# Performance work log

Measured on AMD Instinct MI355X. Metric: run time of the kernel, lower is better.

Reference implementation:

```python
import jax, jax.numpy as jnp
import numpy as np

# config constants
H = 1024          # hidden_size
I = 512           # moe_intermediate_size
IS = 1024         # moe_shared_expert_intermediate_size
E = 16            # n_routed_experts
G = 4             # n_group
TOPK_G = 2        # topk_group
TOPK = 4          # num_experts_per_tok
SCALE = 2.5       # routed_scaling_factor
B, S = 2, 1024


def _relu2(x):
    r = jax.nn.relu(x)
    return r * r


def setup_inputs() -> dict:
    key = jax.random.key(0)
    ks = jax.random.split(key, 8)
    sd = 0.02
    return {
        "hidden_states": jax.random.normal(ks[0], (B, S, H), jnp.float32),
        "Wg": jax.random.normal(ks[1], (E, H), jnp.float32) * sd,          # router gate weight
        "bias_corr": jax.random.normal(ks[2], (E,), jnp.float32) * 0.01,    # e_score_correction_bias
        "W1": jax.random.normal(ks[3], (E, I, H), jnp.float32) * sd,        # experts up_proj
        "W2": jax.random.normal(ks[4], (E, H, I), jnp.float32) * sd,        # experts down_proj
        "Ws1": jax.random.normal(ks[5], (IS, H), jnp.float32) * sd,         # shared up_proj
        "Ws2": jax.random.normal(ks[6], (H, IS), jnp.float32) * sd,         # shared down_proj
    }


def _route(scores, bias_corr):
    # scores: (T,E) = sigmoid(router logits)
    T = scores.shape[0]
    s_choice = scores + bias_corr                                           # (T,E)
    gs = s_choice.reshape(T, G, E // G)
    group_scores = jnp.sum(jax.lax.top_k(gs, 2)[0], axis=-1)                # (T,G) sum of top-2 per group
    gidx = jax.lax.top_k(group_scores, TOPK_G)[1]                           # (T,topk_group)
    gmask = jnp.sum(jax.nn.one_hot(gidx, G, dtype=scores.dtype), axis=1)    # (T,G)
    smask = jnp.repeat(gmask, E // G, axis=1)                               # (T,E)
    masked = jnp.where(smask > 0, s_choice, 0.0)
    topk_idx = jax.lax.top_k(masked, TOPK)[1]                               # (T,top_k)
    topk_w = jnp.take_along_axis(scores, topk_idx, axis=1)                  # weights from raw sigmoid scores
    topk_w = topk_w / (jnp.sum(topk_w, axis=-1, keepdims=True) + 1e-20)     # norm_topk_prob
    topk_w = topk_w * SCALE
    return topk_idx, topk_w


def reference(hidden_states, Wg, bias_corr, W1, W2, Ws1, Ws2):
    b, s, h = hidden_states.shape
    flat = hidden_states.reshape(-1, h)                                     # (T,H)
    T = flat.shape[0]
    logits = flat.astype(jnp.float32) @ Wg.T                                # (T,E)
    scores = jax.nn.sigmoid(logits)
    topk_idx, topk_w = _route(scores, bias_corr)
    topk_w = topk_w.astype(hidden_states.dtype)
    # combined per-(token, expert) weight; zero where not routed (equivalent
    # to the per-expert gather/MLP/weighted index_add in the original)
    cw = jnp.zeros((T, E), flat.dtype)
    cw = cw.at[jnp.arange(T)[:, None], topk_idx].add(topk_w)                # (T,E)
    # fc1_latent_proj / fc2_latent_proj are Identity (moe_latent_size=None)
    hid = _relu2(jnp.einsum('th,eih->eti', flat, W1))                       # (E,T,I)
    y = jnp.einsum('eti,ehi->eth', hid, W2)                                 # (E,T,H)
    out = jnp.einsum('eth,te->th', y, cw)                                   # (T,H)
    shared = _relu2(flat @ Ws1.T) @ Ws2.T                                   # shared expert on residuals
    return (out + shared).reshape(b, s, h)
```

## Files before the change

kernel.cpp:

```cpp
#include <hip/hip_runtime.h>
#include <hip/hip_bf16.h>

#define T_TOK 2048
#define HDIM 1024
#define IDIM 512
#define ISDIM 1024
#define NEXP 16
#define TOPK 4
#define NSLOT (T_TOK*TOPK)
#define SCALE_F 2.5f

typedef unsigned short u16;
typedef float f32x4 __attribute__((ext_vector_type(4)));
typedef __bf16 bf16x8 __attribute__((ext_vector_type(8)));
typedef u16 u16x8 __attribute__((ext_vector_type(8)));

__device__ __forceinline__ u16 f2bf(float f) {
  unsigned u = __builtin_bit_cast(unsigned, f);
  u += 0x7fffu + ((u >> 16) & 1u);
  return (u16)(u >> 16);
}

__device__ __forceinline__ float bf2f(u16 h) {
  unsigned u = ((unsigned)h) << 16;
  return __builtin_bit_cast(float, u);
}

__device__ __forceinline__ void gload_lds16(const u16* g, u16* l) {
  __builtin_amdgcn_global_load_lds(
      (const __attribute__((address_space(1))) void*)g,
      (__attribute__((address_space(3))) void*)l, 16, 0, 0);
}

__device__ __forceinline__ f32x4 mfma16(u16x8 a, u16x8 b, f32x4 c) {
  return __builtin_amdgcn_mfma_f32_16x16x32_bf16(
      __builtin_bit_cast(bf16x8, a), __builtin_bit_cast(bf16x8, b), c, 0, 0, 0);
}

__device__ __forceinline__ void wait_vm6()   { asm volatile("s_waitcnt vmcnt(6)" ::: "memory"); }
__device__ __forceinline__ void wait_vm0()   { asm volatile("s_waitcnt vmcnt(0)" ::: "memory"); }
__device__ __forceinline__ void wait_lgkm0() { asm volatile("s_waitcnt lgkmcnt(0)" ::: "memory"); }

__global__ void __launch_bounds__(256) router_kernel(
    const float* __restrict__ x, const float* __restrict__ Wg,
    const float* __restrict__ bias,
    int* __restrict__ topk_idx, float* __restrict__ topk_w,
    u16* __restrict__ Xbf) {
  int t = blockIdx.x;
  int tid = threadIdx.x;
  int lane = tid & 63;
  int wave = tid >> 6;

  __shared__ __align__(16) float sx[HDIM];
  __shared__ float ssc[NEXP];

  float4 xv = reinterpret_cast<const float4*>(x + (size_t)t * HDIM)[tid];
  reinterpret_cast<float4*>(sx)[tid] = xv;
  ushort4 o;
  o.x = f2bf(xv.x); o.y = f2bf(xv.y); o.z = f2bf(xv.z); o.w = f2bf(xv.w);
  reinterpret_cast<ushort4*>(Xbf + (size_t)t * HDIM)[tid] = o;
  __syncthreads();

  float acc[4] = {0.f, 0.f, 0.f, 0.f};
  const float4* sx4 = reinterpret_cast<const float4*>(sx);
#pragma unroll
  for (int c = 0; c < 4; c++) {
    float4 xq = sx4[lane + 64 * c];
#pragma unroll
    for (int e = 0; e < 4; e++) {
      float4 wq = reinterpret_cast<const float4*>(
          Wg + (size_t)(wave * 4 + e) * HDIM)[lane + 64 * c];
      acc[e] += xq.x * wq.x + xq.y * wq.y + xq.z * wq.z + xq.w * wq.w;
    }
  }
#pragma unroll
  for (int e = 0; e < 4; e++) {
    float v = acc[e];
#pragma unroll
    for (int off = 32; off > 0; off >>= 1) v += __shfl_xor(v, off);
    if (lane == 0) ssc[wave * 4 + e] = v;
  }
  __syncthreads();

  if (tid == 0) {
    float scores[NEXP], sc[NEXP];
#pragma unroll
    for (int e = 0; e < NEXP; e++) {
      float s = 1.f / (1.f + expf(-ssc[e]));
      scores[e] = s;
      sc[e] = s + bias[e];
    }
    float gsum[4];
#pragma unroll
    for (int g = 0; g < 4; g++) {
      float a = sc[4*g], b = sc[4*g+1], c = sc[4*g+2], d = sc[4*g+3];
      float hi1 = fmaxf(a, b), lo1 = fminf(a, b);
      float hi2 = fmaxf(c, d), lo2 = fminf(c, d);
      gsum[g] = fmaxf(hi1, hi2) + fmaxf(fminf(hi1, hi2), fmaxf(lo1, lo2));
    }
    int g0 = 0; float bv = gsum[0];
#pragma unroll
    for (int g = 1; g < 4; g++) if (gsum[g] > bv) { bv = gsum[g]; g0 = g; }
    int g1 = -1; float bv2 = -1e30f;
#pragma unroll
    for (int g = 0; g < 4; g++) if (g != g0 && gsum[g] > bv2) { bv2 = gsum[g]; g1 = g; }
    float m[NEXP];
#pragma unroll
    for (int e = 0; e < NEXP; e++) {
      int g = e >> 2;
      m[e] = (g == g0 || g == g1) ? sc[e] : 0.0f;
    }
    int idx[TOPK]; float w[TOPK];
#pragma unroll
    for (int k = 0; k < TOPK; k++) {
      int bj = 0; float bmv = m[0];
#pragma unroll
      for (int j = 1; j < NEXP; j++) if (m[j] > bmv) { bmv = m[j]; bj = j; }
      idx[k] = bj; w[k] = scores[bj];
#pragma unroll
      for (int j = 0; j < NEXP; j++) m[j] = (j == bj) ? -1e30f : m[j];
    }
    float s4 = w[0] + w[1] + w[2] + w[3] + 1e-20f;
    float inv = SCALE_F / s4;
#pragma unroll
    for (int k = 0; k < TOPK; k++) {
      topk_idx[t * TOPK + k] = idx[k];
      topk_w[t * TOPK + k] = w[k] * inv;
    }
  }
}

__global__ void __launch_bounds__(256) route_build(
    const int* __restrict__ topk_idx, const float* __restrict__ topk_w,
    int* __restrict__ offsets, int* __restrict__ counts,
    int* __restrict__ perm_token, float* __restrict__ perm_w,
    int* __restrict__ slot_of) {
  __shared__ int hcnt[NEXP];
  __shared__ int hfill[NEXP];
  int tid = threadIdx.x;
  if (tid < NEXP) hcnt[tid] = 0;
  __syncthreads();

  int e_loc[NSLOT / 256];
#pragma unroll
  for (int i = 0; i < NSLOT / 256; i++) {
    int j = tid + 256 * i;
    int e = topk_idx[j];
    e_loc[i] = e;
    atomicAdd(&hcnt[e], 1);
  }
  __syncthreads();

  if (tid == 0) {
    int s = 0;
#pragma unroll
    for (int e = 0; e < NEXP; e++) {
      int c = hcnt[e];
      offsets[e] = s;
      counts[e] = c;
      hfill[e] = s;
      s += c;
    }
  }
  __syncthreads();

#pragma unroll
  for (int i = 0; i < NSLOT / 256; i++) {
    int j = tid + 256 * i;
    int pos = atomicAdd(&hfill[e_loc[i]], 1);
    perm_token[pos] = j >> 2;
    perm_w[pos] = topk_w[j];
    slot_of[j] = pos;
  }
}

#define N1Q (NEXP*IDIM*HDIM/4)
#define NSQ (ISDIM*HDIM/4)
__global__ void __launch_bounds__(256) cvt_all(
    const float* __restrict__ W1, const float* __restrict__ W2,
    const float* __restrict__ Ws1, const float* __restrict__ Ws2,
    u16* __restrict__ W1b, u16* __restrict__ W2b,
    u16* __restrict__ Ws1b, u16* __restrict__ Ws2b) {
  int i = blockIdx.x * 256 + threadIdx.x;
  const float* src; u16* dst; int off;
  if (i < N1Q)               { src = W1;  dst = W1b;  off = i; }
  else if (i < 2 * N1Q)      { src = W2;  dst = W2b;  off = i - N1Q; }
  else if (i < 2 * N1Q + NSQ){ src = Ws1; dst = Ws1b; off = i - 2 * N1Q; }
  else                       { src = Ws2; dst = Ws2b; off = i - 2 * N1Q - NSQ; }
  float4 v = reinterpret_cast<const float4*>(src)[off];
  ushort4 o;
  o.x = f2bf(v.x); o.y = f2bf(v.y); o.z = f2bf(v.z); o.w = f2bf(v.w);
  reinterpret_cast<ushort4*>(dst)[off] = o;
}

#define BM 64
#define BN 128
#define BK 64

template<int PHASE>
__global__ void __launch_bounds__(256) moe_gemm(
    const u16* __restrict__ Xbf, const u16* __restrict__ Hg,
    const u16* __restrict__ Hs,
    const u16* __restrict__ W1b, const u16* __restrict__ W2b,
    const u16* __restrict__ Ws1b, const u16* __restrict__ Ws2b,
    const int* __restrict__ eoffs, const int* __restrict__ ecnts,
    const int* __restrict__ rowmap, const float* __restrict__ rowscale,
    u16* __restrict__ HgOut, u16* __restrict__ HsOut,
    u16* __restrict__ Ygb, float* __restrict__ Ys)
{
  constexpr int KL = (PHASE == 0) ? HDIM : IDIM;
  constexpr int NT = KL / BK;

  int flat = blockIdx.x + gridDim.x * (blockIdx.y + gridDim.y * blockIdx.z);
  int chunk = (gridDim.x * gridDim.y * gridDim.z) >> 3;
  int widx = (flat & 7) * chunk + (flat >> 3);
  int mb = widx % gridDim.x;
  int tmp = widx / gridDim.x;
  int nb = tmp % gridDim.y;
  int e  = tmp / gridDim.y;

  bool sh = (e >= NEXP);
  int half = e - NEXP;
  int N, Mloc, rowbase, Astr, Bstr, kb;
  const u16* Abase;
  const u16* Bp;
  if (PHASE == 0) {
    Astr = HDIM; Bstr = HDIM; kb = 0;
    if (sh) { N = ISDIM; Mloc = T_TOK; rowbase = 0; Abase = Xbf; Bp = Ws1b; }
    else    { N = IDIM; Mloc = ecnts[e]; rowbase = eoffs[e]; Abase = Xbf;
              Bp = W1b + (size_t)e * IDIM * HDIM; }
  } else {
    N = HDIM;
    if (sh) { Astr = ISDIM; Bstr = ISDIM; kb = half * IDIM;
              Mloc = T_TOK; rowbase = 0; Abase = Hs; Bp = Ws2b; }
    else    { Astr = IDIM; Bstr = IDIM; kb = 0;
              Mloc = ecnts[e]; rowbase = eoffs[e]; Abase = Hg;
              Bp = W2b + (size_t)e * HDIM * IDIM; }
  }
  int m0 = mb * BM;
  if (m0 >= Mloc) return;
  int n0 = nb * BN;
  if (n0 >= N) return;

  __shared__ __align__(16) u16 sA[2][BM * BK];
  __shared__ __align__(16) u16 sB[2][BN * BK];

  int tid = threadIdx.x;
  int lane = tid & 63;
  int wave = tid >> 6;
  int wm = (wave >> 1) * 32;
  int wn = (wave & 1) * 64;
  int fm = lane & 15;
  int kq = lane >> 4;
  int fsw = fm & 7;

  int lrow8 = lane >> 3;
  int sch = ((lane & 7) ^ lrow8) * 8;

  const u16* AgP[2];
  int aoff[2];
#pragma unroll
  for (int g = 0; g < 2; g++) {
    int rt = 16 * wave + 8 * g + lrow8;
    int ar = m0 + rt;
    int arc = (ar < Mloc) ? ar : (Mloc - 1);
    size_t asrc;
    if (PHASE == 0 && !sh) asrc = (size_t)rowmap[rowbase + arc] * Astr;
    else                   asrc = (size_t)((sh ? 0 : rowbase) + arc) * Astr;
    AgP[g] = Abase + asrc + kb + sch;
    aoff[g] = (16 * wave + 8 * g) * BK;
  }
  const u16* BgP[4];
  int boff[4];
#pragma unroll
  for (int g = 0; g < 4; g++) {
    int rt = 32 * wave + 8 * g + lrow8;
    BgP[g] = Bp + (size_t)(n0 + rt) * Bstr + kb + sch;
    boff[g] = (32 * wave + 8 * g) * BK;
  }

  f32x4 acc[2][4] = {};

#pragma unroll
  for (int g = 0; g < 2; g++) gload_lds16(AgP[g], &sA[0][aoff[g]]);
#pragma unroll
  for (int g = 0; g < 4; g++) gload_lds16(BgP[g], &sB[0][boff[g]]);
#pragma unroll
  for (int g = 0; g < 2; g++) gload_lds16(AgP[g] + BK, &sA[1][aoff[g]]);
#pragma unroll
  for (int g = 0; g < 4; g++) gload_lds16(BgP[g] + BK, &sB[1][boff[g]]);

  for (int t = 0; t < NT - 1; ++t) {
    int cur = t & 1;
    wait_vm6();
    __builtin_amdgcn_s_barrier();
    u16x8 af[2][2], bf[2][4];
#pragma unroll
    for (int ks = 0; ks < 2; ks++) {
      int ch = ((ks * 4 + kq) ^ fsw) * 8;
#pragma unroll
      for (int i = 0; i < 2; i++)
        af[ks][i] = *reinterpret_cast<const u16x8*>(&sA[cur][(wm + 16 * i + fm) * BK + ch]);
#pragma unroll
      for (int j = 0; j < 4; j++)
        bf[ks][j] = *reinterpret_cast<const u16x8*>(&sB[cur][(wn + 16 * j + fm) * BK + ch]);
    }
    wait_lgkm0();
    __builtin_amdgcn_sched_barrier(0);
    __builtin_amdgcn_s_barrier();
    if (t + 2 < NT) {
#pragma unroll
      for (int g = 0; g < 2; g++) gload_lds16(AgP[g] + (t + 2) * BK, &sA[cur][aoff[g]]);
#pragma unroll
      for (int g = 0; g < 4; g++) gload_lds16(BgP[g] + (t + 2) * BK, &sB[cur][boff[g]]);
    }
#pragma unroll
    for (int ks = 0; ks < 2; ks++)
#pragma unroll
      for (int i = 0; i < 2; i++)
#pragma unroll
        for (int j = 0; j < 4; j++)
          acc[i][j] = mfma16(af[ks][i], bf[ks][j], acc[i][j]);
  }
  {
    constexpr int cur = (NT - 1) & 1;
    wait_vm0();
    __builtin_amdgcn_s_barrier();
    u16x8 af[2][2], bf[2][4];
#pragma unroll
    for (int ks = 0; ks < 2; ks++) {
      int ch = ((ks * 4 + kq) ^ fsw) * 8;
#pragma unroll
      for (int i = 0; i < 2; i++)
        af[ks][i] = *reinterpret_cast<const u16x8*>(&sA[cur][(wm + 16 * i + fm) * BK + ch]);
#pragma unroll
      for (int j = 0; j < 4; j++)
        bf[ks][j] = *reinterpret_cast<const u16x8*>(&sB[cur][(wn + 16 * j + fm) * BK + ch]);
    }
    wait_lgkm0();
    __builtin_amdgcn_sched_barrier(0);
#pragma unroll
    for (int ks = 0; ks < 2; ks++)
#pragma unroll
      for (int i = 0; i < 2; i++)
#pragma unroll
        for (int j = 0; j < 4; j++)
          acc[i][j] = mfma16(af[ks][i], bf[ks][j], acc[i][j]);
  }

#pragma unroll
  for (int i = 0; i < 2; i++) {
#pragma unroll
    for (int r = 0; r < 4; r++) {
      int gm = m0 + wm + 16 * i + kq * 4 + r;
      if (gm < Mloc) {
        float rs = 0.f;
        if (PHASE == 0 && !sh) rs = rowscale[rowbase + gm];
#pragma unroll
        for (int j = 0; j < 4; j++) {
          int gn = n0 + wn + 16 * j + fm;
          float v = acc[i][j][r];
          if (PHASE == 0) {
            float tq = fmaxf(v, 0.f);
            if (!sh) {
              tq = tq * tq * rs;
              HgOut[(size_t)(rowbase + gm) * IDIM + gn] = f2bf(tq);
            } else {
              HsOut[(size_t)gm * ISDIM + gn] = f2bf(tq * tq);
            }
          } else {
            if (!sh) Ygb[(size_t)(rowbase + gm) * HDIM + gn] = f2bf(v);
            else     Ys[(size_t)(half * T_TOK + gm) * HDIM + gn] = v;
          }
        }
      }
    }
  }
}

__global__ void __launch_bounds__(256) combine_kernel(
    const u16* __restrict__ Ygb, const float* __restrict__ Ys,
    const int* __restrict__ slot_of, float* __restrict__ out) {
  int t = blockIdx.x;
  int i = threadIdx.x;
  int4 s = *reinterpret_cast<const int4*>(&slot_of[t * 4]);
  const ushort4* Y4 = reinterpret_cast<const ushort4*>(Ygb);
  const float4* S4 = reinterpret_cast<const float4*>(Ys);
  float4* O4 = reinterpret_cast<float4*>(out);
  float4 v0 = S4[(size_t)t * 256 + i];
  float4 v1 = S4[(size_t)(T_TOK + t) * 256 + i];
  ushort4 a = Y4[(size_t)s.x * 256 + i];
  ushort4 b = Y4[(size_t)s.y * 256 + i];
  ushort4 c = Y4[(size_t)s.z * 256 + i];
  ushort4 d = Y4[(size_t)s.w * 256 + i];
  float4 v;
  v.x = v0.x + v1.x + bf2f(a.x) + bf2f(b.x) + bf2f(c.x) + bf2f(d.x);
  v.y = v0.y + v1.y + bf2f(a.y) + bf2f(b.y) + bf2f(c.y) + bf2f(d.y);
  v.z = v0.z + v1.z + bf2f(a.z) + bf2f(b.z) + bf2f(c.z) + bf2f(d.z);
  v.w = v0.w + v1.w + bf2f(a.w) + bf2f(b.w) + bf2f(c.w) + bf2f(d.w);
  O4[(size_t)t * 256 + i] = v;
}

extern "C" void kernel_launch(void* const* d_in, const int* in_sizes, int n_in,
                              void* d_out, int out_size, void* d_ws, size_t ws_size,
                              hipStream_t stream) {
  const float* x    = (const float*)d_in[0];
  const float* Wg   = (const float*)d_in[1];
  const float* bias = (const float*)d_in[2];
  const float* W1   = (const float*)d_in[3];
  const float* W2   = (const float*)d_in[4];
  const float* Ws1  = (const float*)d_in[5];
  const float* Ws2  = (const float*)d_in[6];
  float* out = (float*)d_out;

  char* p = (char*)d_ws;
  auto alloc = [&](size_t bytes) -> void* {
    void* r = (void*)p;
    p += (bytes + 255) & ~(size_t)255;
    return r;
  };
  int*   topk_idx   = (int*)  alloc((size_t)NSLOT * 4);
  float* topk_w     = (float*)alloc((size_t)NSLOT * 4);
  int*   counts     = (int*)  alloc(64);
  int*   offsets    = (int*)  alloc(64);
  int*   perm_token = (int*)  alloc((size_t)NSLOT * 4);
  float* perm_w     = (float*)alloc((size_t)NSLOT * 4);
  int*   slot_of    = (int*)  alloc((size_t)NSLOT * 4);
  u16*   Xbf        = (u16*)  alloc((size_t)T_TOK * HDIM * 2);
  u16*   W1b        = (u16*)  alloc((size_t)NEXP * IDIM * HDIM * 2);
  u16*   W2b        = (u16*)  alloc((size_t)NEXP * HDIM * IDIM * 2);
  u16*   Ws1b      = (u16*)  alloc((size_t)ISDIM * HDIM * 2);
  u16*   Ws2b      = (u16*)  alloc((size_t)HDIM * ISDIM * 2);
  u16*   Hg         = (u16*)  alloc((size_t)NSLOT * IDIM * 2);
  u16*   Hs         = (u16*)  alloc((size_t)T_TOK * ISDIM * 2);
  u16*   Ygb        = (u16*)  alloc((size_t)NSLOT * HDIM * 2);
  float* Ys         = (float*)alloc((size_t)2 * T_TOK * HDIM * 4);

  router_kernel<<<T_TOK, 256, 0, stream>>>(x, Wg, bias, topk_idx, topk_w, Xbf);
  route_build<<<1, 256, 0, stream>>>(topk_idx, topk_w, offsets, counts,
                                     perm_token, perm_w, slot_of);

  cvt_all<<<(2 * N1Q + 2 * NSQ + 255) / 256, 256, 0, stream>>>(
      W1, W2, Ws1, Ws2, W1b, W2b, Ws1b, Ws2b);

  moe_gemm<0><<<dim3(T_TOK / BM, ISDIM / BN, NEXP + 1), 256, 0, stream>>>(
      Xbf, Hg, Hs, W1b, W2b, Ws1b, Ws2b, offsets, counts,
      perm_token, perm_w, Hg, Hs, nullptr, nullptr);

  moe_gemm<1><<<dim3(T_TOK / BM, HDIM / BN, NEXP + 2), 256, 0, stream>>>(
      Xbf, Hg, Hs, W1b, W2b, Ws1b, Ws2b, offsets, counts,
      perm_token, perm_w, Hg, Hs, Ygb, Ys);

  combine_kernel<<<T_TOK, 256, 0, stream>>>(Ygb, Ys, slot_of, out);
}
```

Baseline: 257.3 us.

## Build compact load-balanced tile lists for MoE GEMMs instead of dense grids

The route-building kernel now produces explicit per-phase tile lists. Shared-expert tiles and only the occupied routed-expert M-tiles are greedily assigned across 8 XCD buckets to balance load. The GEMM kernels read their tile code from the list instead of decoding a dense 3D grid that was mostly empty blocks. This removes launches of idle workgroups and evens out work across XCDs. It adds serial single-thread scheduling work in route_build, and the tile lists have fixed capacities that must not overflow.

```diff
diff --git a/kernel.cpp b/kernel.cpp
--- a/kernel.cpp
+++ b/kernel.cpp
@@ -40,6 +40,11 @@
 __device__ __forceinline__ void wait_vm6()   { asm volatile("s_waitcnt vmcnt(6)" ::: "memory"); }
 __device__ __forceinline__ void wait_vm0()   { asm volatile("s_waitcnt vmcnt(0)" ::: "memory"); }
 __device__ __forceinline__ void wait_lgkm0() { asm volatile("s_waitcnt lgkmcnt(0)" ::: "memory"); }
+
+#define JMAX0 136
+#define G0T (8*JMAX0)
+#define JMAX1 240
+#define G1T (8*JMAX1)
 
 __global__ void __launch_bounds__(256) router_kernel(
     const float* __restrict__ x, const float* __restrict__ Wg,
@@ -134,7 +139,8 @@
     const int* __restrict__ topk_idx, const float* __restrict__ topk_w,
     int* __restrict__ offsets, int* __restrict__ counts,
     int* __restrict__ perm_token, float* __restrict__ perm_w,
-    int* __restrict__ slot_of) {
+    int* __restrict__ slot_of,
+    int* __restrict__ tiles0, int* __restrict__ tiles1) {
   __shared__ int hcnt[NEXP];
   __shared__ int hfill[NEXP];
   int tid = threadIdx.x;
@@ -171,6 +177,52 @@
     perm_token[pos] = j >> 2;
     perm_w[pos] = topk_w[j];
     slot_of[j] = pos;
+  }
+
+  for (int i = tid; i < G0T; i += 256) tiles0[i] = -1;
+  for (int i = tid; i < G1T; i += 256) tiles1[i] = -1;
+  __syncthreads();
+
+  if (tid == 0) {
+    int load[8] = {0,0,0,0,0,0,0,0};
+    for (int nb = 0; nb < 8; nb++) {
+      int x = 0;
+      for (int q = 1; q < 8; q++) if (load[q] < load[x]) x = q;
+      for (int mb = 0; mb < 32; mb++)
+        tiles0[x + 8 * (load[x]++)] = (16 << 10) | (mb << 3) | nb;
+    }
+    for (int e = 0; e < NEXP; e++) {
+      int mc = (hcnt[e] + 63) >> 6;
+      for (int nb = 0; nb < 4; nb++)
+        for (int base = 0; base < mc; base += 32) {
+          int cn = min(32, mc - base);
+          int x = 0;
+          for (int q = 1; q < 8; q++) if (load[q] < load[x]) x = q;
+          for (int mm = 0; mm < cn; mm++)
+            tiles0[x + 8 * (load[x]++)] = (e << 10) | ((base + mm) << 3) | nb;
+        }
+    }
+  }
+  if (tid == 1) {
+    int load[8] = {0,0,0,0,0,0,0,0};
+    for (int eh = 16; eh <= 17; eh++)
+      for (int nb = 0; nb < 8; nb++) {
+        int x = 0;
+        for (int q = 1; q < 8; q++) if (load[q] < load[x]) x = q;
+        for (int mb = 0; mb < 32; mb++)
+          tiles1[x + 8 * (load[x]++)] = (eh << 10) | (mb << 3) | nb;
+      }
+    for (int e = 0; e < NEXP; e++) {
+      int mc = (hcnt[e] + 63) >> 6;
+      for (int nb = 0; nb < 8; nb++)
+        for (int base = 0; base < mc; base += 32) {
+          int cn = min(32, mc - base);
+          int x = 0;
+          for (int q = 1; q < 8; q++) if (load[q] < load[x]) x = q;
+          for (int mm = 0; mm < cn; mm++)
+            tiles1[x + 8 * (load[x]++)] = (e << 10) | ((base + mm) << 3) | nb;
+        }
+    }
   }
 }
 
@@ -199,6 +251,7 @@
 
 template<int PHASE>
 __global__ void __launch_bounds__(256) moe_gemm(
+    const int* __restrict__ tiles,
     const u16* __restrict__ Xbf, const u16* __restrict__ Hg,
     const u16* __restrict__ Hs,
     const u16* __restrict__ W1b, const u16* __restrict__ W2b,
@@ -211,13 +264,11 @@
   constexpr int KL = (PHASE == 0) ? HDIM : IDIM;
   constexpr int NT = KL / BK;
 
-  int flat = blockIdx.x + gridDim.x * (blockIdx.y + gridDim.y * blockIdx.z);
-  int chunk = (gridDim.x * gridDim.y * gridDim.z) >> 3;
-  int widx = (flat & 7) * chunk + (flat >> 3);
-  int mb = widx % gridDim.x;
-  int tmp = widx / gridDim.x;
-  int nb = tmp % gridDim.y;
-  int e  = tmp / gridDim.y;
+  int code = tiles[blockIdx.x];
+  if (code < 0) return;
+  int e  = code >> 10;
+  int mb = (code >> 3) & 127;
+  int nb = code & 7;
 
   bool sh = (e >= NEXP);
   int half = e - NEXP;
@@ -426,6 +477,8 @@
   int*   perm_token = (int*)  alloc((size_t)NSLOT * 4);
   float* perm_w     = (float*)alloc((size_t)NSLOT * 4);
   int*   slot_of    = (int*)  alloc((size_t)NSLOT * 4);
+  int*   tiles0     = (int*)  alloc((size_t)G0T * 4);
+  int*   tiles1     = (int*)  alloc((size_t)G1T * 4);
   u16*   Xbf        = (u16*)  alloc((size_t)T_TOK * HDIM * 2);
   u16*   W1b        = (u16*)  alloc((size_t)NEXP * IDIM * HDIM * 2);
   u16*   W2b        = (u16*)  alloc((size_t)NEXP * HDIM * IDIM * 2);
@@ -438,17 +491,18 @@
 
   router_kernel<<<T_TOK, 256, 0, stream>>>(x, Wg, bias, topk_idx, topk_w, Xbf);
   route_build<<<1, 256, 0, stream>>>(topk_idx, topk_w, offsets, counts,
-                                     perm_token, perm_w, slot_of);
+                                     perm_token, perm_w, slot_of,
+                                     tiles0, tiles1);
 
   cvt_all<<<(2 * N1Q + 2 * NSQ + 255) / 256, 256, 0, stream>>>(
       W1, W2, Ws1, Ws2, W1b, W2b, Ws1b, Ws2b);
 
-  moe_gemm<0><<<dim3(T_TOK / BM, ISDIM / BN, NEXP + 1), 256, 0, stream>>>(
-      Xbf, Hg, Hs, W1b, W2b, Ws1b, Ws2b, offsets, counts,
+  moe_gemm<0><<<G0T, 256, 0, stream>>>(
+      tiles0, Xbf, Hg, Hs, W1b, W2b, Ws1b, Ws2b, offsets, counts,
       perm_token, perm_w, Hg, Hs, nullptr, nullptr);
 
-  moe_gemm<1><<<dim3(T_TOK / BM, HDIM / BN, NEXP + 2), 256, 0, stream>>>(
-      Xbf, Hg, Hs, W1b, W2b, Ws1b, Ws2b, offsets, counts,
+  moe_gemm<1><<<G1T, 256, 0, stream>>>(
+      tiles1, Xbf, Hg, Hs, W1b, W2b, Ws1b, Ws2b, offsets, counts,
       perm_token, perm_w, Hg, Hs, Ygb, Ys);
 
   combine_kernel<<<T_TOK, 256, 0, stream>>>(Ygb, Ys, slot_of, out);
```

After: 436.7 us. 69.8% more time.
